# Kernel tuning notes

Measured on AMD Instinct MI355X. Metric: run time of the kernel, lower is better.

Reference implementation:

```python
import jax, jax.numpy as jnp
import numpy as np

EPS = 1e-12  # matches torch F.normalize clamp_min eps


def agnn_conv(x, src, dst, beta, num_nodes):
    # x: [N, H]; src/dst: [E'] (self-loops already included)
    norm = jnp.sqrt(jnp.sum(x * x, axis=-1, keepdims=True))
    x_norm = x / jnp.maximum(norm, EPS)
    # edge-wise cosine similarity scaled by beta
    logits = beta * jnp.sum(x_norm[src] * x_norm[dst], axis=-1)  # [E']
    # scatter-softmax over incoming edges of each destination node
    m = jax.ops.segment_max(logits, dst, num_segments=num_nodes)  # [N]
    e = jnp.exp(logits - m[dst])
    s = jax.ops.segment_sum(e, dst, num_segments=num_nodes)       # [N]
    alpha = e / s[dst]                                            # [E']
    # weighted scatter-add aggregation of source features
    return jax.ops.segment_sum(alpha[:, None] * x[src], dst, num_segments=num_nodes)


def setup_inputs() -> dict:
    key = jax.random.key(0)
    ks = jax.random.split(key, 8)
    N, E, C_in, C_hid, C_out = 100000, 1600000, 512, 128, 64
    x = jax.random.normal(ks[0], (N, C_in), dtype=jnp.float32)
    edge_index = jax.random.randint(ks[1], (2, E), 0, N, dtype=jnp.int64)
    W1 = jax.random.normal(ks[2], (C_in, C_hid), dtype=jnp.float32) / np.sqrt(C_in)
    b1 = jnp.zeros((C_hid,), dtype=jnp.float32)
    W2 = jax.random.normal(ks[3], (C_hid, C_out), dtype=jnp.float32) / np.sqrt(C_hid)
    b2 = jnp.zeros((C_out,), dtype=jnp.float32)
    beta2 = jnp.array(1.0, dtype=jnp.float32)  # learned beta of prop2; prop1 beta fixed at 1.0
    return {"x": x, "edge_index": edge_index, "W1": W1, "b1": b1,
            "beta2": beta2, "W2": W2, "b2": b2}


def reference(x, edge_index, W1, b1, beta2, W2, b2):
    N = x.shape[0]
    # AGNNConv adds self-loops by default
    loops = jnp.arange(N, dtype=edge_index.dtype)
    src = jnp.concatenate([edge_index[0], loops])
    dst = jnp.concatenate([edge_index[1], loops])
    # dropout is identity in eval mode
    h = jax.nn.relu(x @ W1 + b1)                      # [N, hidden]
    h = agnn_conv(h, src, dst, jnp.float32(1.0), N)   # prop1 (beta frozen = 1)
    h = agnn_conv(h, src, dst, beta2, N)              # prop2 (learned beta)
    logits = h @ W2 + b2                              # [N, out]
    return jax.nn.log_softmax(logits, axis=1)
```

## Files before the change

### kernel.cpp

```cpp
#include <hip/hip_runtime.h>
#include <math.h>


static inline int divup(int a, int b) { return (a + b - 1) / b; }

typedef __attribute__((ext_vector_type(8))) short short8;
typedef __attribute__((ext_vector_type(4))) float f32x4;
union U16 { uint4 u; short8 s; };

__device__ __forceinline__ unsigned bf16r(float f) {
    unsigned u = __float_as_uint(f);
    return (u + 0x7FFFu + ((u >> 16) & 1u)) >> 16;
}
__device__ __forceinline__ unsigned pack2(float a, float b) {
    return bf16r(a) | (bf16r(b) << 16);
}
__device__ __forceinline__ float bflo(unsigned u) { return __uint_as_float(u << 16); }
__device__ __forceinline__ float bfhi(unsigned u) { return __uint_as_float(u & 0xFFFF0000u); }

__global__ __launch_bounds__(64) void k_detect(const int* __restrict__ raw, int* flag) {
    int t = threadIdx.x;
    int v = raw[2 * t + 1];
    unsigned long long b = __ballot(v != 0);
    if (t == 0) *flag = (b == 0ULL) ? 1 : 0;
}

__global__ __launch_bounds__(256) void k_cvt(const int* __restrict__ raw, int E,
                                             const int* __restrict__ flag,
                                             int* __restrict__ s32, int* __restrict__ d32,
                                             int* __restrict__ cnt) {
    int i = blockIdx.x * blockDim.x + threadIdx.x;
    if (i >= E) return;
    int s, d;
    if (*flag) {
        s = raw[2 * (size_t)i];
        d = raw[2 * ((size_t)E + i)];
    } else {
        s = raw[i];
        d = raw[(size_t)E + i];
    }
    s32[i] = s;
    d32[i] = d;
    atomicAdd(&cnt[d], 1);
}

__global__ __launch_bounds__(1024) void k_scan1(const int* __restrict__ cnt, int N,
                                                int* __restrict__ rp, int* __restrict__ bsum) {
    __shared__ int sm[1024];
    int t = threadIdx.x;
    int i = blockIdx.x * 1024 + t;
    int v = (i < N) ? cnt[i] + 1 : 0;
    sm[t] = v;
    __syncthreads();
#pragma unroll
    for (int off = 1; off < 1024; off <<= 1) {
        int u = (t >= off) ? sm[t - off] : 0;
        __syncthreads();
        sm[t] += u;
        __syncthreads();
    }
    if (i < N) rp[i] = sm[t] - v;
    if (t == 1023) bsum[blockIdx.x] = sm[t];
}

__global__ __launch_bounds__(64) void k_scan2(int* __restrict__ bsum, int nb) {
    if (threadIdx.x == 0) {
        int run = 0;
        for (int i = 0; i < nb; ++i) { int v = bsum[i]; bsum[i] = run; run += v; }
    }
}

__global__ __launch_bounds__(256) void k_scan3(int* __restrict__ rp, const int* __restrict__ bsum,
                                               int N, int Etot, int* __restrict__ cursor) {
    int i = blockIdx.x * blockDim.x + threadIdx.x;
    if (i < N) {
        int v = rp[i] + bsum[i >> 10];
        rp[i] = v;
        cursor[i] = v;
    } else if (i == N) {
        rp[N] = Etot;
    }
}

__global__ __launch_bounds__(256) void k_scatter(const int* __restrict__ s32,
                                                 const int* __restrict__ d32, int E, int N,
                                                 int* __restrict__ cursor,
                                                 int* __restrict__ esrc) {
    int b = blockIdx.x;
    int xcd = b & 7;
    int nstripe = gridDim.x >> 3;
    int stripe = b >> 3;
    int lo = (int)(((long long)xcd * N) >> 3);
    int hi = (int)(((long long)(xcd + 1) * N) >> 3);
    int Etot = E + N;
    for (int e = stripe * 256 + threadIdx.x; e < Etot; e += nstripe * 256) {
        int d = (e < E) ? d32[e] : (e - E);
        if (d < lo || d >= hi) continue;
        int s = (e < E) ? s32[e] : d;
        int pos = atomicAdd(&cursor[d], 1);
        esrc[pos] = s;
    }
}

__global__ __launch_bounds__(256) void k_cvtW1(const float* __restrict__ W1,
                                               unsigned short* __restrict__ W1t) {
    int i = blockIdx.x * 256 + threadIdx.x;
    if (i >= 512 * 128) return;
    int k = i >> 7, n = i & 127;
    W1t[n * 512 + k] = (unsigned short)bf16r(W1[i]);
}

__global__ __launch_bounds__(256) void k_cvtW2(const float* __restrict__ W2,
                                               unsigned short* __restrict__ W2t) {
    int i = blockIdx.x * 256 + threadIdx.x;
    if (i >= 128 * 64) return;
    int k = i >> 6, n = i & 63;
    W2t[n * 128 + k] = (unsigned short)bf16r(W2[i]);
}

#define XS(row, off) ((off) ^ (((row) & 7) << 4))
__global__ __launch_bounds__(256) void k_gemm1(const float* __restrict__ x,
                                               const unsigned short* __restrict__ W1t,
                                               const float* __restrict__ b1, int N,
                                               unsigned short* __restrict__ xh1,
                                               float* __restrict__ n1) {
    __shared__ __align__(16) unsigned char lds[33792];
    const int tid = threadIdx.x;
    const int lane = tid & 63;
    const int lt = lane & 15, lg = lane >> 4;
    const int wid = tid >> 6;
    const int wr = wid >> 1, wc = wid & 1;
    const int row0 = blockIdx.x * 128;
    const int arow = tid >> 1, ahalf = tid & 1;

    f32x4 acc[4][4];
#pragma unroll
    for (int i = 0; i < 4; ++i)
#pragma unroll
        for (int j = 0; j < 4; ++j) acc[i][j] = (f32x4){0.f, 0.f, 0.f, 0.f};

    float4 av[8];
    uint4 bv[4];
    const int grow = row0 + arow;
    const bool aok = grow < N;

    auto issue = [&](int k0) {
        const float* xp = x + (size_t)grow * 512 + k0 + ahalf * 32;
#pragma unroll
        for (int i = 0; i < 8; ++i)
            av[i] = aok ? ((const float4*)xp)[i] : make_float4(0.f, 0.f, 0.f, 0.f);
        const unsigned short* wp = W1t + (size_t)arow * 512 + k0 + ahalf * 32;
#pragma unroll
        for (int i = 0; i < 4; ++i) bv[i] = ((const uint4*)wp)[i];
    };
    auto commit = [&]() {
        unsigned char* ab = lds + arow * 128;
#pragma unroll
        for (int i = 0; i < 4; ++i) {
            uint4 q;
            q.x = pack2(av[2 * i].x, av[2 * i].y);
            q.y = pack2(av[2 * i].z, av[2 * i].w);
            q.z = pack2(av[2 * i + 1].x, av[2 * i + 1].y);
            q.w = pack2(av[2 * i + 1].z, av[2 * i + 1].w);
            *(uint4*)(ab + XS(arow, ahalf * 64 + i * 16)) = q;
        }
        unsigned char* bb = lds + 16384 + arow * 128;
#pragma unroll
        for (int i = 0; i < 4; ++i)
            *(uint4*)(bb + XS(arow, ahalf * 64 + i * 16)) = bv[i];
    };

    issue(0);
    commit();
    __syncthreads();

    for (int t = 0; t < 8; ++t) {
        if (t < 7) issue((t + 1) * 64);
#pragma unroll
        for (int sub = 0; sub < 2; ++sub) {
            U16 af[4], bf[4];
#pragma unroll
            for (int mi = 0; mi < 4; ++mi) {
                int r = wr * 64 + mi * 16 + lt;
                af[mi].u = *(const uint4*)(lds + r * 128 + XS(r, sub * 64 + lg * 16));
            }
#pragma unroll
            for (int ni = 0; ni < 4; ++ni) {
                int r = wc * 64 + ni * 16 + lt;
                bf[ni].u = *(const uint4*)(lds + 16384 + r * 128 + XS(r, sub * 64 + lg * 16));
            }
#pragma unroll
            for (int mi = 0; mi < 4; ++mi)
#pragma unroll
                for (int ni = 0; ni < 4; ++ni)
                    acc[mi][ni] = __builtin_amdgcn_mfma_f32_16x16x32_bf16(
                        af[mi].s, bf[ni].s, acc[mi][ni], 0, 0, 0);
        }
        __syncthreads();
        if (t < 7) {
            commit();
            __syncthreads();
        }
    }

    float bias[4];
#pragma unroll
    for (int ni = 0; ni < 4; ++ni) bias[ni] = b1[wc * 64 + ni * 16 + lt];
    float* sc = (float*)lds;
#pragma unroll 1
    for (int c = 0; c < 2; ++c) {
        __syncthreads();
        if (wr == c) {
#pragma unroll
            for (int mi = 0; mi < 4; ++mi)
#pragma unroll
                for (int reg = 0; reg < 4; ++reg) {
                    int rl = mi * 16 + lg * 4 + reg;
#pragma unroll
                    for (int ni = 0; ni < 4; ++ni)
                        sc[rl * 132 + wc * 64 + ni * 16 + lt] =
                            fmaxf(acc[mi][ni][reg] + bias[ni], 0.f);
                }
        }
        __syncthreads();
        {
            int rl = tid >> 2, q = tid & 3;
            int gr = row0 + c * 64 + rl;
            const float* rowp = sc + rl * 132 + q * 32;
            float v[32];
#pragma unroll
            for (int i = 0; i < 8; ++i) {
                float4 f = ((const float4*)rowp)[i];
                v[4 * i] = f.x; v[4 * i + 1] = f.y; v[4 * i + 2] = f.z; v[4 * i + 3] = f.w;
            }
            float s2 = 0.f;
#pragma unroll
            for (int i = 0; i < 32; ++i) s2 += v[i] * v[i];
            s2 += __shfl_xor(s2, 1, 64);
            s2 += __shfl_xor(s2, 2, 64);
            float nrm = sqrtf(s2);
            float rn = 1.0f / fmaxf(nrm, 1e-12f);
            if (gr < N) {
                uint4 o[4];
                unsigned* op = (unsigned*)o;
#pragma unroll
                for (int i = 0; i < 16; ++i)
                    op[i] = pack2(v[2 * i] * rn, v[2 * i + 1] * rn);
                uint4* dst = (uint4*)(xh1 + (size_t)gr * 128 + q * 32);
                dst[0] = o[0];
                dst[1] = o[1];
                dst[2] = o[2];
                dst[3] = o[3];
                if (q == 0) n1[gr] = nrm;
            }
        }
    }
}

__global__ __launch_bounds__(256) void k_conv(const unsigned short* __restrict__ xh,
                                              const float* __restrict__ nrmt,
                                              const int* __restrict__ rp,
                                              const int* __restrict__ esrc, int N,
                                              const float* __restrict__ betap,
                                              unsigned short* __restrict__ outh,
                                              float* __restrict__ outn) {
    int node = (blockIdx.x * blockDim.x + threadIdx.x) >> 6;
    if (node >= N) return;
    int lane = threadIdx.x & 63;
    int t = lane & 15, g = lane >> 4;
    float beta = betap ? *betap : 1.0f;

    uint4 hdu = *(const uint4*)&xh[(size_t)node * 128 + 8 * t];
    float hd[8];
    hd[0] = bflo(hdu.x); hd[1] = bfhi(hdu.x);
    hd[2] = bflo(hdu.y); hd[3] = bfhi(hdu.y);
    hd[4] = bflo(hdu.z); hd[5] = bfhi(hdu.z);
    hd[6] = bflo(hdu.w); hd[7] = bfhi(hdu.w);

    int e0 = rp[node], e1 = rp[node + 1];
    float acc[8] = {0.f, 0.f, 0.f, 0.f, 0.f, 0.f, 0.f, 0.f};
    float ssum = 0.f;

    for (int eb = e0; eb < e1; eb += 4) {
        int e = eb + g;
        int ee = (e < e1) ? e : e0;
        int s = esrc[ee];
        float ns = nrmt[s];
        uint4 hu = *(const uint4*)&xh[(size_t)s * 128 + 8 * t];
        float v[8];
        v[0] = bflo(hu.x); v[1] = bfhi(hu.x);
        v[2] = bflo(hu.y); v[3] = bfhi(hu.y);
        v[4] = bflo(hu.z); v[5] = bfhi(hu.z);
        v[6] = bflo(hu.w); v[7] = bfhi(hu.w);
        float p = 0.f;
#pragma unroll
        for (int j = 0; j < 8; ++j) p += v[j] * hd[j];
        p += __shfl_xor(p, 1, 64);
        p += __shfl_xor(p, 2, 64);
        p += __shfl_xor(p, 4, 64);
        p += __shfl_xor(p, 8, 64);
        float w = (e < e1) ? __expf(p * beta) : 0.f;
        float wn = w * ns;
        ssum += w;
#pragma unroll
        for (int j = 0; j < 8; ++j) acc[j] += wn * v[j];
    }
#pragma unroll
    for (int j = 0; j < 8; ++j) {
        acc[j] += __shfl_xor(acc[j], 16, 64);
        acc[j] += __shfl_xor(acc[j], 32, 64);
    }
    ssum += __shfl_xor(ssum, 16, 64);
    ssum += __shfl_xor(ssum, 32, 64);
    float r = 1.0f / ssum;

    if (outn == nullptr) {
        if (g == 0) {
            uint4 q;
            q.x = pack2(acc[0] * r, acc[1] * r);
            q.y = pack2(acc[2] * r, acc[3] * r);
            q.z = pack2(acc[4] * r, acc[5] * r);
            q.w = pack2(acc[6] * r, acc[7] * r);
            *(uint4*)&outh[(size_t)node * 128 + 8 * t] = q;
        }
    } else {
        float o[8];
        float s2 = 0.f;
#pragma unroll
        for (int j = 0; j < 8; ++j) { o[j] = acc[j] * r; s2 += o[j] * o[j]; }
        s2 += __shfl_xor(s2, 1, 64);
        s2 += __shfl_xor(s2, 2, 64);
        s2 += __shfl_xor(s2, 4, 64);
        s2 += __shfl_xor(s2, 8, 64);
        float nn = sqrtf(s2);
        float rn = 1.0f / fmaxf(nn, 1e-12f);
        if (g == 0) {
            uint4 q;
            q.x = pack2(o[0] * rn, o[1] * rn);
            q.y = pack2(o[2] * rn, o[3] * rn);
            q.z = pack2(o[4] * rn, o[5] * rn);
            q.w = pack2(o[6] * rn, o[7] * rn);
            *(uint4*)&outh[(size_t)node * 128 + 8 * t] = q;
            if (t == 0) outn[node] = nn;
        }
    }
}

#define G2_ASTRIDE 272
__global__ __launch_bounds__(256) void k_gemm2(const unsigned short* __restrict__ h,
                                               const unsigned short* __restrict__ W2t,
                                               const float* __restrict__ b2, int N,
                                               float* __restrict__ out) {
    __shared__ __align__(16) unsigned char As[128 * G2_ASTRIDE];
    __shared__ __align__(16) unsigned char Bs[64 * G2_ASTRIDE];
    const int tid = threadIdx.x;
    const int lane = tid & 63;
    const int lt = lane & 15, lg = lane >> 4;
    const int wid = tid >> 6;
    const int row0 = blockIdx.x * 128;

    {
        int arow = tid >> 1, ahalf = tid & 1;
        const uint4* src = (const uint4*)(h + (size_t)(row0 + arow) * 128 + ahalf * 64);
        unsigned char* ab = As + arow * G2_ASTRIDE + ahalf * 128;
#pragma unroll
        for (int i = 0; i < 8; ++i) ((uint4*)ab)[i] = src[i];
        int brow = tid >> 2, bq = tid & 3;
        const uint4* bs = (const uint4*)(W2t + (size_t)brow * 128 + bq * 32);
        unsigned char* bb = Bs + brow * G2_ASTRIDE + bq * 64;
#pragma unroll
        for (int i = 0; i < 4; ++i) ((uint4*)bb)[i] = bs[i];
    }
    __syncthreads();

    f32x4 acc[2][4];
#pragma unroll
    for (int i = 0; i < 2; ++i)
#pragma unroll
        for (int j = 0; j < 4; ++j) acc[i][j] = (f32x4){0.f, 0.f, 0.f, 0.f};

#pragma unroll
    for (int sub = 0; sub < 4; ++sub) {
        U16 af[2], bf[4];
#pragma unroll
        for (int mi = 0; mi < 2; ++mi)
            af[mi].u = *(const uint4*)(As + (wid * 32 + mi * 16 + lt) * G2_ASTRIDE + sub * 64 + lg * 16);
#pragma unroll
        for (int ni = 0; ni < 4; ++ni)
            bf[ni].u = *(const uint4*)(Bs + (ni * 16 + lt) * G2_ASTRIDE + sub * 64 + lg * 16);
#pragma unroll
        for (int mi = 0; mi < 2; ++mi)
#pragma unroll
            for (int ni = 0; ni < 4; ++ni)
                acc[mi][ni] = __builtin_amdgcn_mfma_f32_16x16x32_bf16(
                    af[mi].s, bf[ni].s, acc[mi][ni], 0, 0, 0);
    }

    float bias[4];
#pragma unroll
    for (int ni = 0; ni < 4; ++ni) bias[ni] = b2[ni * 16 + lt];

#pragma unroll
    for (int mi = 0; mi < 2; ++mi) {
#pragma unroll
        for (int reg = 0; reg < 4; ++reg) {
            int row = row0 + wid * 32 + mi * 16 + lg * 4 + reg;
            if (row < N) {
                float v[4];
#pragma unroll
                for (int ni = 0; ni < 4; ++ni) v[ni] = acc[mi][ni][reg] + bias[ni];
                float m = fmaxf(fmaxf(v[0], v[1]), fmaxf(v[2], v[3]));
                m = fmaxf(m, __shfl_xor(m, 1, 64));
                m = fmaxf(m, __shfl_xor(m, 2, 64));
                m = fmaxf(m, __shfl_xor(m, 4, 64));
                m = fmaxf(m, __shfl_xor(m, 8, 64));
                float s = __expf(v[0] - m) + __expf(v[1] - m) +
                          __expf(v[2] - m) + __expf(v[3] - m);
                s += __shfl_xor(s, 1, 64);
                s += __shfl_xor(s, 2, 64);
                s += __shfl_xor(s, 4, 64);
                s += __shfl_xor(s, 8, 64);
                float lg2 = logf(s);
#pragma unroll
                for (int ni = 0; ni < 4; ++ni)
                    out[(size_t)row * 64 + ni * 16 + lt] = v[ni] - m - lg2;
            }
        }
    }
}

extern "C" void kernel_launch(void* const* d_in, const int* in_sizes, int n_in,
                              void* d_out, int out_size, void* d_ws, size_t ws_size,
                              hipStream_t stream) {
    const float* x     = (const float*)d_in[0];
    const int*   ei    = (const int*)d_in[1];
    const float* W1    = (const float*)d_in[2];
    const float* b1    = (const float*)d_in[3];
    const float* beta2 = (const float*)d_in[4];
    const float* W2    = (const float*)d_in[5];
    const float* b2    = (const float*)d_in[6];
    float* out = (float*)d_out;

    const int N = in_sizes[0] / 512;
    const int E = in_sizes[1] / 2;
    const int Etot = E + N;

    char* ws = (char*)d_ws;
    size_t off = 0;
    auto alloc = [&](size_t bytes) -> void* {
        void* p = ws + off;
        off = (off + bytes + 511) & ~(size_t)511;
        return p;
    };
    unsigned short* t1 = (unsigned short*)alloc((size_t)N * 128 * 2);
    unsigned short* t2 = (unsigned short*)alloc((size_t)N * 128 * 2);
    float* n1   = (float*)alloc((size_t)N * 4);
    float* n2   = (float*)alloc((size_t)N * 4);
    int* cnt    = (int*)alloc((size_t)N * 4);
    int* rp     = (int*)alloc((size_t)(N + 1) * 4);
    int* cursor = (int*)alloc((size_t)N * 4);
    int* bsum   = (int*)alloc(4096);
    int* flag   = (int*)alloc(512);
    unsigned short* W1t = (unsigned short*)alloc(512 * 128 * 2);
    unsigned short* W2t = (unsigned short*)alloc(128 * 64 * 2);
    int* s32    = (int*)alloc((size_t)E * 4);
    int* d32    = (int*)alloc((size_t)E * 4);
    int* esrc   = (int*)alloc((size_t)Etot * 4);
    (void)ws_size; (void)n_in; (void)out_size;

    (void)hipMemsetAsync(cnt, 0, (size_t)N * 4, stream);

    k_detect<<<1, 64, 0, stream>>>(ei, flag);
    k_cvt<<<divup(E, 256), 256, 0, stream>>>(ei, E, flag, s32, d32, cnt);
    int nb = divup(N, 1024);
    k_scan1<<<nb, 1024, 0, stream>>>(cnt, N, rp, bsum);
    k_scan2<<<1, 64, 0, stream>>>(bsum, nb);
    k_scan3<<<divup(N + 1, 256), 256, 0, stream>>>(rp, bsum, N, Etot, cursor);
    k_scatter<<<2048, 256, 0, stream>>>(s32, d32, E, N, cursor, esrc);

    k_cvtW1<<<divup(512 * 128, 256), 256, 0, stream>>>(W1, W1t);
    k_cvtW2<<<divup(128 * 64, 256), 256, 0, stream>>>(W2, W2t);

    k_gemm1<<<divup(N, 128), 256, 0, stream>>>(x, W1t, b1, N, t1, n1);
    k_conv<<<divup(N, 4), 256, 0, stream>>>(t1, n1, rp, esrc, N, nullptr, t2, n2);
    k_conv<<<divup(N, 4), 256, 0, stream>>>(t2, n2, rp, esrc, N, beta2, t1, nullptr);
    k_gemm2<<<divup(N, 128), 256, 0, stream>>>(t1, W2t, b2, N, out);
}
```

Measured before the change: 453.7 us.

## Restructure GEMM1 to stream x from registers and stage W1 per half-K in LDS

The first GEMM no longer stages x tiles through LDS. Each wave loads its own 32 rows of x directly into registers with a one-step prefetch, converts them to bf16 in place, and feeds MFMA against a 128x256 W1 half staged in LDS with a column swizzle. This removes the per-k-tile LDS round trip and most of the barriers, at the cost of more accumulator registers per wave and a larger LDS allocation. The epilogue now packs the normalized bf16 rows into LDS first and writes them out as fully coalesced 16-byte stores.

```diff
diff --git a/kernel.cpp b/kernel.cpp
--- a/kernel.cpp
+++ b/kernel.cpp
@@ -118,114 +118,113 @@
     W2t[n * 128 + k] = (unsigned short)bf16r(W2[i]);
 }
 
-#define XS(row, off) ((off) ^ (((row) & 7) << 4))
+#define XSW(c, off) ((off) ^ (((c) & 7) << 4))
 __global__ __launch_bounds__(256) void k_gemm1(const float* __restrict__ x,
                                                const unsigned short* __restrict__ W1t,
                                                const float* __restrict__ b1, int N,
                                                unsigned short* __restrict__ xh1,
                                                float* __restrict__ n1) {
-    __shared__ __align__(16) unsigned char lds[33792];
+    __shared__ __align__(16) unsigned char lds[65536];
     const int tid = threadIdx.x;
     const int lane = tid & 63;
     const int lt = lane & 15, lg = lane >> 4;
-    const int wid = tid >> 6;
-    const int wr = wid >> 1, wc = wid & 1;
+    const int w = tid >> 6;
     const int row0 = blockIdx.x * 128;
-    const int arow = tid >> 1, ahalf = tid & 1;
-
-    f32x4 acc[4][4];
-#pragma unroll
-    for (int i = 0; i < 4; ++i)
-#pragma unroll
-        for (int j = 0; j < 4; ++j) acc[i][j] = (f32x4){0.f, 0.f, 0.f, 0.f};
-
-    float4 av[8];
-    uint4 bv[4];
-    const int grow = row0 + arow;
-    const bool aok = grow < N;
-
-    auto issue = [&](int k0) {
-        const float* xp = x + (size_t)grow * 512 + k0 + ahalf * 32;
-#pragma unroll
-        for (int i = 0; i < 8; ++i)
-            av[i] = aok ? ((const float4*)xp)[i] : make_float4(0.f, 0.f, 0.f, 0.f);
-        const unsigned short* wp = W1t + (size_t)arow * 512 + k0 + ahalf * 32;
-#pragma unroll
-        for (int i = 0; i < 4; ++i) bv[i] = ((const uint4*)wp)[i];
-    };
-    auto commit = [&]() {
-        unsigned char* ab = lds + arow * 128;
-#pragma unroll
-        for (int i = 0; i < 4; ++i) {
-            uint4 q;
-            q.x = pack2(av[2 * i].x, av[2 * i].y);
-            q.y = pack2(av[2 * i].z, av[2 * i].w);
-            q.z = pack2(av[2 * i + 1].x, av[2 * i + 1].y);
-            q.w = pack2(av[2 * i + 1].z, av[2 * i + 1].w);
-            *(uint4*)(ab + XS(arow, ahalf * 64 + i * 16)) = q;
-        }
-        unsigned char* bb = lds + 16384 + arow * 128;
-#pragma unroll
-        for (int i = 0; i < 4; ++i)
-            *(uint4*)(bb + XS(arow, ahalf * 64 + i * 16)) = bv[i];
-    };
-
-    issue(0);
-    commit();
-    __syncthreads();
-
-    for (int t = 0; t < 8; ++t) {
-        if (t < 7) issue((t + 1) * 64);
-#pragma unroll
-        for (int sub = 0; sub < 2; ++sub) {
-            U16 af[4], bf[4];
-#pragma unroll
-            for (int mi = 0; mi < 4; ++mi) {
-                int r = wr * 64 + mi * 16 + lt;
-                af[mi].u = *(const uint4*)(lds + r * 128 + XS(r, sub * 64 + lg * 16));
-            }
-#pragma unroll
-            for (int ni = 0; ni < 4; ++ni) {
-                int r = wc * 64 + ni * 16 + lt;
-                bf[ni].u = *(const uint4*)(lds + 16384 + r * 128 + XS(r, sub * 64 + lg * 16));
-            }
-#pragma unroll
-            for (int mi = 0; mi < 4; ++mi)
-#pragma unroll
-                for (int ni = 0; ni < 4; ++ni)
-                    acc[mi][ni] = __builtin_amdgcn_mfma_f32_16x16x32_bf16(
-                        af[mi].s, bf[ni].s, acc[mi][ni], 0, 0, 0);
-        }
-        __syncthreads();
-        if (t < 7) {
-            commit();
-            __syncthreads();
-        }
-    }
-
-    float bias[4];
-#pragma unroll
-    for (int ni = 0; ni < 4; ++ni) bias[ni] = b1[wc * 64 + ni * 16 + lt];
+
+    const float* xb[2];
+#pragma unroll
+    for (int rf = 0; rf < 2; ++rf) {
+        int r = row0 + w * 32 + rf * 16 + lt;
+        if (r > N - 1) r = N - 1;
+        xb[rf] = x + (size_t)r * 512 + lg * 8;
+    }
+
+    f32x4 acc[2][8];
+#pragma unroll
+    for (int i = 0; i < 2; ++i)
+#pragma unroll
+        for (int j = 0; j < 8; ++j) acc[i][j] = (f32x4){0.f, 0.f, 0.f, 0.f};
+
+    for (int ph = 0; ph < 2; ++ph) {
+        const int kb = ph * 256;
+        float4 ac[2][2], an[2][2];
+#pragma unroll
+        for (int rf = 0; rf < 2; ++rf) {
+            ac[rf][0] = ((const float4*)(xb[rf] + kb))[0];
+            ac[rf][1] = ((const float4*)(xb[rf] + kb))[1];
+        }
+        __syncthreads();
+        {
+            int c = tid >> 1, h = tid & 1;
+            const uint4* wp = (const uint4*)(W1t + c * 512 + kb + h * 128);
+            unsigned char* base = lds + c * 512;
+#pragma unroll
+            for (int i = 0; i < 16; ++i)
+                *(uint4*)(base + XSW(c, h * 256 + i * 16)) = wp[i];
+        }
+        __syncthreads();
+
+#pragma unroll
+        for (int ks = 0; ks < 8; ++ks) {
+            if (ks < 7) {
+#pragma unroll
+                for (int rf = 0; rf < 2; ++rf) {
+                    an[rf][0] = ((const float4*)(xb[rf] + kb + (ks + 1) * 32))[0];
+                    an[rf][1] = ((const float4*)(xb[rf] + kb + (ks + 1) * 32))[1];
+                }
+            }
+            U16 af[2];
+#pragma unroll
+            for (int rf = 0; rf < 2; ++rf) {
+                af[rf].u.x = pack2(ac[rf][0].x, ac[rf][0].y);
+                af[rf].u.y = pack2(ac[rf][0].z, ac[rf][0].w);
+                af[rf].u.z = pack2(ac[rf][1].x, ac[rf][1].y);
+                af[rf].u.w = pack2(ac[rf][1].z, ac[rf][1].w);
+            }
+#pragma unroll
+            for (int cf = 0; cf < 8; ++cf) {
+                int col = cf * 16 + lt;
+                U16 bf;
+                bf.u = *(const uint4*)(lds + col * 512 + XSW(col, ks * 64 + lg * 16));
+#pragma unroll
+                for (int rf = 0; rf < 2; ++rf)
+                    acc[rf][cf] = __builtin_amdgcn_mfma_f32_16x16x32_bf16(
+                        af[rf].s, bf.s, acc[rf][cf], 0, 0, 0);
+            }
+            if (ks < 7) {
+#pragma unroll
+                for (int rf = 0; rf < 2; ++rf) {
+                    ac[rf][0] = an[rf][0];
+                    ac[rf][1] = an[rf][1];
+                }
+            }
+        }
+    }
+
+    float bias[8];
+#pragma unroll
+    for (int cf = 0; cf < 8; ++cf) bias[cf] = b1[cf * 16 + lt];
     float* sc = (float*)lds;
+    unsigned char* pk = lds + 36864;
 #pragma unroll 1
-    for (int c = 0; c < 2; ++c) {
-        __syncthreads();
-        if (wr == c) {
-#pragma unroll
-            for (int mi = 0; mi < 4; ++mi)
+    for (int p = 0; p < 2; ++p) {
+        __syncthreads();
+        if ((w >> 1) == p) {
+#pragma unroll
+            for (int rf = 0; rf < 2; ++rf)
 #pragma unroll
                 for (int reg = 0; reg < 4; ++reg) {
-                    int rl = mi * 16 + lg * 4 + reg;
-#pragma unroll
-                    for (int ni = 0; ni < 4; ++ni)
-                        sc[rl * 132 + wc * 64 + ni * 16 + lt] =
-                            fmaxf(acc[mi][ni][reg] + bias[ni], 0.f);
+                    int rl = (w & 1) * 32 + rf * 16 + lg * 4 + reg;
+#pragma unroll
+                    for (int cf = 0; cf < 8; ++cf)
+                        sc[rl * 132 + cf * 16 + lt] =
+                            fmaxf(acc[rf][cf][reg] + bias[cf], 0.f);
                 }
         }
         __syncthreads();
         {
             int rl = tid >> 2, q = tid & 3;
-            int gr = row0 + c * 64 + rl;
+            int gr = row0 + p * 64 + rl;
             const float* rowp = sc + rl * 132 + q * 32;
             float v[32];
 #pragma unroll
@@ -240,19 +239,24 @@
             s2 += __shfl_xor(s2, 2, 64);
             float nrm = sqrtf(s2);
             float rn = 1.0f / fmaxf(nrm, 1e-12f);
-            if (gr < N) {
-                uint4 o[4];
-                unsigned* op = (unsigned*)o;
-#pragma unroll
-                for (int i = 0; i < 16; ++i)
-                    op[i] = pack2(v[2 * i] * rn, v[2 * i + 1] * rn);
-                uint4* dst = (uint4*)(xh1 + (size_t)gr * 128 + q * 32);
-                dst[0] = o[0];
-                dst[1] = o[1];
-                dst[2] = o[2];
-                dst[3] = o[3];
-                if (q == 0) n1[gr] = nrm;
-            }
+            uint4 o[4];
+            unsigned* op = (unsigned*)o;
+#pragma unroll
+            for (int i = 0; i < 16; ++i)
+                op[i] = pack2(v[2 * i] * rn, v[2 * i + 1] * rn);
+            uint4* pd = (uint4*)(pk + rl * 256 + q * 64);
+            pd[0] = o[0]; pd[1] = o[1]; pd[2] = o[2]; pd[3] = o[3];
+            if (q == 0 && gr < N) n1[gr] = nrm;
+        }
+        __syncthreads();
+#pragma unroll
+        for (int j = 0; j < 4; ++j) {
+            int boff = j * 4096 + tid * 16;
+            int r = boff >> 8;
+            int gr = row0 + p * 64 + r;
+            if (gr < N)
+                *(uint4*)((unsigned char*)xh1 + (size_t)gr * 256 + (boff & 255)) =
+                    *(const uint4*)(pk + boff);
         }
     }
 }
```

After: 435.5 us. 1.04x faster.
